# Performance work log

Hardware: AMD Instinct MI355X
Metric: run time of the kernel (lower is better)

## Reference

```python
import jax, jax.numpy as jnp
import numpy as np

B, C, H, S, E, NH, DD, DS = 16, 256, 1024, 1024, 512, 8, 512, 64
HD = E // NH               # head dim = 64
REL_MAX = 2048             # seq_len + prediction_length
S1 = S + 1                 # dyn tokens + 1 static token
NEG = jnp.float32(-1e9)


def setup_inputs() -> dict:
    key = jax.random.key(0)
    ks = jax.random.split(key, 24)
    rn = lambda k, shp, s=0.02: (jax.random.normal(k, shp, jnp.float32) * s)
    return {
        # forward tensor args
        "x":      jax.random.normal(ks[0], (B, C, H), jnp.float32),
        "dyn":    jax.random.normal(ks[1], (B, S, DD), jnp.float32),
        "static": jax.random.normal(ks[2], (B, DS), jnp.float32),
        # dynamic/static encoders (nn.Linear: y = x @ W.T + b)
        "dyn_W":  rn(ks[3], (E, DD)),  "dyn_b":  jnp.zeros((E,), jnp.float32),
        "stat_W": rn(ks[4], (E, DS)),  "stat_b": jnp.zeros((E,), jnp.float32),
        # static FiLM MLP: Linear(E,E) -> LeakyReLU(0.1) -> Linear(E,C) -> Tanh
        "film_W1": rn(ks[5], (E, E)), "film_b1": jnp.zeros((E,), jnp.float32),
        "film_W2": rn(ks[6], (C, E)), "film_b2": jnp.zeros((C,), jnp.float32),
        # query_proj: Conv1d(C->E, k=1)  (weight stored as [E, C])
        "q_W": rn(ks[7], (E, C)), "q_b": jnp.zeros((E,), jnp.float32),
        # MultiheadAttention packed in-proj [3E, E] and out-proj [E, E]
        "in_proj_W": rn(ks[8], (3 * E, E)), "in_proj_b": jnp.zeros((3 * E,), jnp.float32),
        "out_W": rn(ks[9], (E, E)), "out_b": jnp.zeros((E,), jnp.float32),
        # context_proj: Conv1d(E->C, k=1) (weight stored as [C, E])
        "ctx_W": rn(ks[10], (C, E)), "ctx_b": jnp.zeros((C,), jnp.float32),
        # learned relative-position bias table, size 2*REL_MAX-1
        "bias_table": rn(ks[11], (2 * REL_MAX - 1,)),
    }


def _leaky(v):
    return jnp.where(v >= 0, v, 0.1 * v)


def _attn_mask(bias_table):
    """Fused relative-position bias + causal mask, shape [H, S1]."""
    q_ids = jnp.arange(H)[:, None]           # [H,1]
    k_ids = jnp.arange(S1)[None, :]          # [1,S1]
    rel = jnp.clip(q_ids - k_ids, -REL_MAX + 1, REL_MAX - 1)
    bias = bias_table[rel + REL_MAX - 1]     # [H,S1]
    # dynamic tokens: query q may attend dyn token j only if j <= min(q, S-1);
    # last (static) token always visible
    allowed = jnp.minimum(q_ids, S - 1)
    blocked = (k_ids < S) & (k_ids > allowed)
    return bias + jnp.where(blocked, NEG, 0.0)


def reference(x, dyn, static, dyn_W, dyn_b, stat_W, stat_b,
              film_W1, film_b1, film_W2, film_b2, q_W, q_b,
              in_proj_W, in_proj_b, out_W, out_b, ctx_W, ctx_b, bias_table):
    # encoders
    dyn_tokens = dyn @ dyn_W.T + dyn_b                      # [B,S,E]
    static_token = static @ stat_W.T + stat_b               # [B,E]
    film = jnp.tanh(_leaky(static_token @ film_W1.T + film_b1) @ film_W2.T + film_b2)  # [B,C]
    cond_tokens = jnp.concatenate([dyn_tokens, static_token[:, None, :]], axis=1)      # [B,S1,E]

    # query_proj (1x1 conv) : [B,C,H] -> [B,H,E]
    query = jnp.einsum('bch,ec->bhe', x, q_W) + q_b

    # multi-head cross-attention with additive mask
    Wq, Wk, Wv = in_proj_W[:E], in_proj_W[E:2 * E], in_proj_W[2 * E:]
    bq, bk, bv = in_proj_b[:E], in_proj_b[E:2 * E], in_proj_b[2 * E:]
    q = (query @ Wq.T + bq).reshape(B, H, NH, HD).transpose(0, 2, 1, 3)        # [B,NH,H,HD]
    k = (cond_tokens @ Wk.T + bk).reshape(B, S1, NH, HD).transpose(0, 2, 1, 3)  # [B,NH,S1,HD]
    v = (cond_tokens @ Wv.T + bv).reshape(B, S1, NH, HD).transpose(0, 2, 1, 3)

    mask = _attn_mask(bias_table)                                               # [H,S1]
    scores = jnp.einsum('bnqd,bnkd->bnqk', q, k) / jnp.sqrt(jnp.float32(HD)) + mask
    attn = jax.nn.softmax(scores, axis=-1)
    ctx = jnp.einsum('bnqk,bnkd->bnqd', attn, v)                                # [B,NH,H,HD]
    ctx = ctx.transpose(0, 2, 1, 3).reshape(B, H, E) @ out_W.T + out_b          # [B,H,E]

    cond_context = jnp.swapaxes(ctx, 1, 2)                                      # [B,E,H]
    cond_residual = jnp.einsum('beh,ce->bch', cond_context, ctx_W) + ctx_b[None, :, None]
    scale = (1.0 + film)[:, :, None]                                            # FiLM [B,C,1]
    x_cond = (x + cond_residual) * scale                                        # == x*s + res*s
    return x_cond
```

## Files before the change

kernel.cpp:

```cpp
#include <hip/hip_runtime.h>
#include <cmath>

#define B_  16
#define C_  256
#define H_  1024
#define S_  1024
#define E_  512
#define NH_ 8
#define DD_ 512
#define DS_ 64
#define HD_ 64
#define S1_ 1025
#define RELM 2048
#define SV  1032

typedef __attribute__((ext_vector_type(8))) short bf16x8;
typedef __attribute__((ext_vector_type(4))) float f32x4;

__device__ __forceinline__ unsigned short f2bf(float f) {
    unsigned u = __float_as_uint(f);
    u += 0x7fffu + ((u >> 16) & 1u);
    return (unsigned short)(u >> 16);
}

__device__ __forceinline__ void gl2lds16(const unsigned short* g, unsigned short* l) {
#if __has_builtin(__builtin_amdgcn_global_load_lds)
    __builtin_amdgcn_global_load_lds(
        (const __attribute__((address_space(1))) void*)g,
        (__attribute__((address_space(3))) void*)l, 16, 0, 0);
#else
    const int ln = threadIdx.x & 63;
    *(bf16x8*)(l + ln * 8) = *(const bf16x8*)g;
#endif
}

__device__ __forceinline__ void conv8(const float* __restrict__ src,
                                      unsigned short* __restrict__ dst, int i) {
    float4 a = *(const float4*)(src + i);
    float4 b = *(const float4*)(src + i + 4);
    bf16x8 o;
    ((unsigned short*)&o)[0] = f2bf(a.x); ((unsigned short*)&o)[1] = f2bf(a.y);
    ((unsigned short*)&o)[2] = f2bf(a.z); ((unsigned short*)&o)[3] = f2bf(a.w);
    ((unsigned short*)&o)[4] = f2bf(b.x); ((unsigned short*)&o)[5] = f2bf(b.y);
    ((unsigned short*)&o)[6] = f2bf(b.z); ((unsigned short*)&o)[7] = f2bf(b.w);
    *(bf16x8*)(dst + i) = o;
}

__device__ __forceinline__ float wred(float p) {
#pragma unroll
    for (int off = 32; off; off >>= 1) p += __shfl_down(p, off, 64);
    return p;
}

#define U_DYN 1048576
#define U_KV  1114112
#define U_Q   1146880
#define U_TOT 1163264
__global__ __launch_bounds__(512)
void prep_conv(const float* __restrict__ dyn, unsigned short* __restrict__ dyn16,
               const float* __restrict__ ipW, unsigned short* __restrict__ ipWq16,
               unsigned short* __restrict__ ipWkv16,
               const float* __restrict__ ctxW, unsigned short* __restrict__ ctxW16,
               const float* __restrict__ statIn,
               const float* __restrict__ stat_W, const float* __restrict__ stat_b,
               float* __restrict__ st_g, unsigned short* __restrict__ st16)
{
    const int blk = blockIdx.x;
    const int t = threadIdx.x;
    if (blk < 512) {
        const float* ipWkv = ipW + (size_t)E_ * E_;
        const int stride = 512 * 512;
        for (int u = blk * 512 + t; u < U_TOT; u += stride) {
            if (u < U_DYN)      conv8(dyn,   dyn16,   u * 8);
            else if (u < U_KV)  conv8(ipWkv, ipWkv16, (u - U_DYN) * 8);
            else if (u < U_Q)   conv8(ipW,   ipWq16,  (u - U_KV) * 8);
            else                conv8(ctxW,  ctxW16,  (u - U_Q) * 8);
        }
    } else {
        const int sub = blk - 512;
        const int b = sub >> 2;
        const int q = sub & 3;
        const int wv = t >> 6;
        const int ln = t & 63;
        const float sv = statIn[b * DS_ + ln];
#pragma unroll 4
        for (int i = 0; i < 16; i++) {
            const int r = q * 128 + wv * 16 + i;
            const float p = wred(stat_W[(size_t)r * DS_ + ln] * sv);
            if (ln == 0) {
                const float v = p + stat_b[r];
                st_g[(size_t)b * E_ + r] = v;
                st16[(size_t)b * E_ + r] = f2bf(v);
            }
        }
    }
}

__global__ __launch_bounds__(512)
void prep_misc(const float* __restrict__ ipW, const float* __restrict__ ipb,
               const float* __restrict__ ctxW,
               const float* __restrict__ q_W, unsigned short* __restrict__ qWT16,
               const float* __restrict__ dynW, unsigned short* __restrict__ dynWT16,
               const float* __restrict__ outW, unsigned short* __restrict__ outWT16,
               const float* __restrict__ q_b, float* __restrict__ qb2,
               const float* __restrict__ dyn_b, float* __restrict__ bkv2,
               const float* __restrict__ out_b, const float* __restrict__ ctx_b,
               float* __restrict__ cb2,
               const float* __restrict__ st_g,
               const float* __restrict__ fW1, const float* __restrict__ fb1,
               float* __restrict__ h1_g)
{
    __shared__ float tle[64][65];
    const int blk = blockIdx.x;
    const int t = threadIdx.x;
    const float* ipWkv = ipW + (size_t)E_ * E_;
    const float* ipbkv = ipb + E_;

    if (blk < 128) {
        const int b   = blk >> 3;
        const int oct = blk & 7;
        const int wv  = t >> 6;
        const int ln  = t & 63;
        float str[8];
        *(float4*)&str[0] = *(const float4*)&st_g[(size_t)b * E_ + ln * 8];
        *(float4*)&str[4] = *(const float4*)&st_g[(size_t)b * E_ + ln * 8 + 4];
#pragma unroll 2
        for (int i = 0; i < 8; i++) {
            const int r = oct * 64 + wv * 8 + i;
            const float* wr = fW1 + (size_t)r * E_ + ln * 8;
            const float4 a = *(const float4*)wr;
            const float4 c = *(const float4*)(wr + 4);
            float p = a.x * str[0] + a.y * str[1] + a.z * str[2] + a.w * str[3]
                    + c.x * str[4] + c.y * str[5] + c.z * str[6] + c.w * str[7];
            p = wred(p);
            if (ln == 0) {
                const float v = p + fb1[r];
                h1_g[(size_t)b * E_ + r] = (v >= 0.f) ? v : 0.1f * v;
            }
        }
    } else if (blk < 352) {
        const int row = (blk - 128) * 8 + (t >> 6);
        const int ln  = t & 63;
        const float* src; const float* vec; float bias; float* dst;
        if (row < 512)       { src = ipW + (size_t)row * E_;            vec = q_b;   bias = ipb[row];        dst = qb2 + row; }
        else if (row < 1536) { const int n = row - 512;  src = ipWkv + (size_t)n * E_; vec = dyn_b; bias = ipbkv[n]; dst = bkv2 + n; }
        else                 { const int n = row - 1536; src = ctxW + (size_t)n * E_;  vec = out_b; bias = ctx_b[n]; dst = cb2 + n; }
        const float4 a  = *(const float4*)(src + ln * 8);
        const float4 c  = *(const float4*)(src + ln * 8 + 4);
        const float4 va = *(const float4*)(vec + ln * 8);
        const float4 vc = *(const float4*)(vec + ln * 8 + 4);
        float p = a.x * va.x + a.y * va.y + a.z * va.z + a.w * va.w
                + c.x * vc.x + c.y * vc.y + c.z * vc.z + c.w * vc.w;
        p = wred(p);
        if (ln == 0) *dst = p + bias;
    } else {
        const float* src; unsigned short* dst; int R, Cc, tile;
        const int tt = blk - 352;
        if (tt < 32)      { src = q_W;  dst = qWT16;   R = 512; Cc = 256; tile = tt; }
        else if (tt < 96) { src = dynW; dst = dynWT16; R = 512; Cc = 512; tile = tt - 32; }
        else              { src = outW; dst = outWT16; R = 512; Cc = 512; tile = tt - 96; }
        const int tpr = Cc / 64;
        const int r0 = (tile / tpr) * 64;
        const int c0 = (tile % tpr) * 64;
        const int tx = t & 15, ty = t >> 4;
#pragma unroll
        for (int i = 0; i < 2; i++) {
            const float4 v = *(const float4*)&src[(size_t)(r0 + ty + i * 32) * Cc + c0 + tx * 4];
            tle[ty + i * 32][tx * 4 + 0] = v.x;
            tle[ty + i * 32][tx * 4 + 1] = v.y;
            tle[ty + i * 32][tx * 4 + 2] = v.z;
            tle[ty + i * 32][tx * 4 + 3] = v.w;
        }
        __syncthreads();
#pragma unroll
        for (int i = 0; i < 2; i++) {
            const int cc = ty + i * 32;
            ushort4 o;
            o.x = f2bf(tle[tx * 4 + 0][cc]);
            o.y = f2bf(tle[tx * 4 + 1][cc]);
            o.z = f2bf(tle[tx * 4 + 2][cc]);
            o.w = f2bf(tle[tx * 4 + 3][cc]);
            *(ushort4*)&dst[(size_t)(c0 + cc) * R + r0 + tx * 4] = o;
        }
    }
}

__global__ __launch_bounds__(256)
void gemm_fold3(const unsigned short* __restrict__ ipWq16, const unsigned short* __restrict__ qWT16,
                unsigned short* __restrict__ WqW16,
                const unsigned short* __restrict__ ipWkv16, const unsigned short* __restrict__ dynWT16,
                unsigned short* __restrict__ Wkv216,
                const unsigned short* __restrict__ ctxW16, const unsigned short* __restrict__ outWT16,
                unsigned short* __restrict__ M216,
                const float* __restrict__ h1_g,
                const float* __restrict__ fW2, const float* __restrict__ fb2,
                float* __restrict__ scaleB)
{
    __shared__ unsigned short At[128 * 32];
    __shared__ unsigned short Wt[128 * 32];
    const int bid = blockIdx.x;
    const int tid  = threadIdx.x;
    if (bid >= 48) {
        const int sub = bid - 48;
        const int b = sub >> 2;
        const int q = sub & 3;
        const int wv = tid >> 6;
        const int ln = tid & 63;
        float h1r[8];
        *(float4*)&h1r[0] = *(const float4*)&h1_g[(size_t)b * E_ + ln * 8];
        *(float4*)&h1r[4] = *(const float4*)&h1_g[(size_t)b * E_ + ln * 8 + 4];
#pragma unroll 2
        for (int i = 0; i < 16; i++) {
            const int c = q * 64 + wv * 16 + i;
            const float* wr = fW2 + (size_t)c * E_ + ln * 8;
            const float4 a = *(const float4*)wr;
            const float4 cc = *(const float4*)(wr + 4);
            float p = a.x * h1r[0] + a.y * h1r[1] + a.z * h1r[2] + a.w * h1r[3]
                    + cc.x * h1r[4] + cc.y * h1r[5] + cc.z * h1r[6] + cc.w * h1r[7];
            p = wred(p);
            if (ln == 0) scaleB[b * C_ + c] = 1.f + tanhf(p + fb2[c]);
        }
        return;
    }
    const unsigned short *A, *W; unsigned short* O; int N, mb, nb;
    if (bid < 8)       { A = ipWq16;  W = qWT16;   O = WqW16;  N = 256; mb = bid >> 1;       nb = bid & 1; }
    else if (bid < 40) { A = ipWkv16; W = dynWT16; O = Wkv216; N = 512; mb = (bid - 8) >> 2; nb = (bid - 8) & 3; }
    else               { A = ctxW16;  W = outWT16; O = M216;   N = 512; mb = (bid - 40) >> 2; nb = (bid - 40) & 3; }
    const int m0 = mb * 128, n0 = nb * 128;

    const int wave = tid >> 6;
    const int lane = tid & 63;
    const int quad = lane >> 4;
    const int l15  = lane & 15;
    const int rw = (wave >> 1) * 64;
    const int cw = (wave & 1) * 64;
    const int srow = lane >> 2;
    const int scol = (lane & 3) * 8;

    f32x4 acc[4][4] = {};
    for (int k0 = 0; k0 < 512; k0 += 32) {
        __syncthreads();
#pragma unroll
        for (int c = 0; c < 2; c++) {
            const int chunk = wave + c * 4;
            gl2lds16(A + (size_t)(m0 + chunk * 16 + srow) * 512 + k0 + scol, &At[chunk * 512]);
            gl2lds16(W + (size_t)(n0 + chunk * 16 + srow) * 512 + k0 + scol, &Wt[chunk * 512]);
        }
        __syncthreads();
        bf16x8 af[4], wf[4];
#pragma unroll
        for (int i = 0; i < 4; i++)
            af[i] = *(const bf16x8*)&At[(rw + i * 16 + l15) * 32 + quad * 8];
#pragma unroll
        for (int j = 0; j < 4; j++)
            wf[j] = *(const bf16x8*)&Wt[(cw + j * 16 + l15) * 32 + quad * 8];
#pragma unroll
        for (int i = 0; i < 4; i++)
#pragma unroll
            for (int j = 0; j < 4; j++)
                acc[i][j] = __builtin_amdgcn_mfma_f32_16x16x32_bf16(af[i], wf[j], acc[i][j], 0, 0, 0);
    }
#pragma unroll
    for (int i = 0; i < 4; i++)
#pragma unroll
        for (int r = 0; r < 4; r++) {
            const int mm = m0 + rw + i * 16 + quad * 4 + r;
            unsigned short* cp = O + (size_t)mm * N + n0 + cw + l15;
#pragma unroll
            for (int j = 0; j < 4; j++)
                cp[j * 16] = f2bf(acc[i][j][r]);
        }
}

__global__ __launch_bounds__(256)
void xpose_kernel(const float* __restrict__ x, unsigned short* __restrict__ xT)
{
    __shared__ float t[64][65];
    const int b = blockIdx.z;
    const int h0 = blockIdx.x * 64;
    const int c0 = blockIdx.y * 64;
    const int tx = threadIdx.x & 15;
    const int ty = threadIdx.x >> 4;
#pragma unroll
    for (int i = 0; i < 4; i++) {
        const float4 v = *(const float4*)&x[((size_t)(b * C_ + c0 + ty + i * 16)) * H_ + h0 + tx * 4];
        t[ty + i * 16][tx * 4 + 0] = v.x;
        t[ty + i * 16][tx * 4 + 1] = v.y;
        t[ty + i * 16][tx * 4 + 2] = v.z;
        t[ty + i * 16][tx * 4 + 3] = v.w;
    }
    __syncthreads();
#pragma unroll
    for (int i = 0; i < 4; i++) {
        const int hh = ty + i * 16;
        ushort4 o;
        o.x = f2bf(t[tx * 4 + 0][hh]);
        o.y = f2bf(t[tx * 4 + 1][hh]);
        o.z = f2bf(t[tx * 4 + 2][hh]);
        o.w = f2bf(t[tx * 4 + 3][hh]);
        *(ushort4*)&xT[((size_t)(b * H_ + h0 + hh)) * C_ + c0 + tx * 4] = o;
    }
}

template<bool FINAL>
__global__ __launch_bounds__(256)
void gemm_mfma(const unsigned short* __restrict__ A, const unsigned short* __restrict__ W,
               const float* __restrict__ bias, void* __restrict__ Cout,
               int M, int N, int K,
               const float* __restrict__ x, const float* __restrict__ scale)
{
    __shared__ unsigned short At[128 * 32];
    __shared__ unsigned short Wt[128 * 32];
    const int tid  = threadIdx.x;
    const int wave = tid >> 6;
    const int lane = tid & 63;
    const int quad = lane >> 4;
    const int l15  = lane & 15;
    const int m0 = blockIdx.y * 128;
    const int n0 = blockIdx.x * 128;
    const int rw = (wave >> 1) * 64;
    const int cw = (wave & 1) * 64;
    const int zb = FINAL ? blockIdx.z : 0;
    const unsigned short* Wb = FINAL ? W + (size_t)zb * N * K : W;

    const int srow = lane >> 2;
    const int scol = (lane & 3) * 8;

    f32x4 acc[4][4] = {};

    for (int k0 = 0; k0 < K; k0 += 32) {
        __syncthreads();
#pragma unroll
        for (int c = 0; c < 2; c++) {
            const int chunk = wave + c * 4;
            gl2lds16(A  + (size_t)(m0 + chunk * 16 + srow) * K + k0 + scol, &At[chunk * 512]);
            gl2lds16(Wb + (size_t)(n0 + chunk * 16 + srow) * K + k0 + scol, &Wt[chunk * 512]);
        }
        __syncthreads();
        bf16x8 af[4], wf[4];
#pragma unroll
        for (int i = 0; i < 4; i++)
            af[i] = *(const bf16x8*)&At[(rw + i * 16 + l15) * 32 + quad * 8];
#pragma unroll
        for (int j = 0; j < 4; j++)
            wf[j] = *(const bf16x8*)&Wt[(cw + j * 16 + l15) * 32 + quad * 8];
#pragma unroll
        for (int i = 0; i < 4; i++)
#pragma unroll
            for (int j = 0; j < 4; j++)
                acc[i][j] = __builtin_amdgcn_mfma_f32_16x16x32_bf16(af[i], wf[j], acc[i][j], 0, 0, 0);
    }

    if constexpr (!FINAL) {
        float bias4[4];
#pragma unroll
        for (int j = 0; j < 4; j++) bias4[j] = bias[n0 + cw + j * 16 + l15];
#pragma unroll
        for (int i = 0; i < 4; i++) {
#pragma unroll
            for (int r = 0; r < 4; r++) {
                const int mm = m0 + rw + i * 16 + quad * 4 + r;
                if (mm < M) {
                    unsigned short* cp = (unsigned short*)Cout + (size_t)mm * N + n0 + cw + l15;
#pragma unroll
                    for (int j = 0; j < 4; j++)
                        cp[j * 16] = f2bf(acc[i][j][r] + bias4[j]);
                }
            }
        }
    } else {
#pragma unroll
        for (int i = 0; i < 4; i++) {
#pragma unroll
            for (int r = 0; r < 4; r++) {
                const int mm = m0 + rw + i * 16 + quad * 4 + r;
                const float cb = bias[mm];
                const float sc = scale[zb * C_ + mm];
                const size_t base = ((size_t)(zb * C_ + mm)) * H_ + n0 + cw + l15;
#pragma unroll
                for (int j = 0; j < 4; j++)
                    ((float*)Cout)[base + j * 16] = (x[base + j * 16] + acc[i][j][r] + cb) * sc;
            }
        }
    }
}

__global__ __launch_bounds__(256)
void gemm_kv(const unsigned short* __restrict__ dynA, const unsigned short* __restrict__ stA,
             const unsigned short* __restrict__ Wdyn, const unsigned short* __restrict__ Wst,
             const float* __restrict__ bdyn, const float* __restrict__ bst,
             unsigned short* __restrict__ k16, unsigned short* __restrict__ vtmp)
{
    __shared__ unsigned short At[128 * 32];
    __shared__ unsigned short Wt[128 * 32];
    const bool stat = (blockIdx.y == 128);
    const unsigned short* A = stat ? stA : dynA;
    const unsigned short* W = stat ? Wst : Wdyn;
    const float* bias = stat ? bst : bdyn;
    const int m0 = stat ? 0 : blockIdx.y * 128;
    const int n0 = blockIdx.x * 128;

    const int tid  = threadIdx.x;
    const int wave = tid >> 6;
    const int lane = tid & 63;
    const int quad = lane >> 4;
    const int l15  = lane & 15;
    const int rw = (wave >> 1) * 64;
    const int cw = (wave & 1) * 64;
    const int srow = lane >> 2;
    const int scol = (lane & 3) * 8;

    f32x4 acc[4][4] = {};
    for (int k0 = 0; k0 < 512; k0 += 32) {
        __syncthreads();
#pragma unroll
        for (int c = 0; c < 2; c++) {
            const int chunk = wave + c * 4;
            gl2lds16(A + (size_t)(m0 + chunk * 16 + srow) * 512 + k0 + scol, &At[chunk * 512]);
            gl2lds16(W + (size_t)(n0 + chunk * 16 + srow) * 512 + k0 + scol, &Wt[chunk * 512]);
        }
        __syncthreads();
        bf16x8 af[4], wf[4];
#pragma unroll
        for (int i = 0; i < 4; i++)
            af[i] = *(const bf16x8*)&At[(rw + i * 16 + l15) * 32 + quad * 8];
#pragma unroll
        for (int j = 0; j < 4; j++)
            wf[j] = *(const bf16x8*)&Wt[(cw + j * 16 + l15) * 32 + quad * 8];
#pragma unroll
        for (int i = 0; i < 4; i++)
#pragma unroll
            for (int j = 0; j < 4; j++)
                acc[i][j] = __builtin_amdgcn_mfma_f32_16x16x32_bf16(af[i], wf[j], acc[i][j], 0, 0, 0);
    }

    const bool isV = (n0 >= 512);
    unsigned short* base = isV ? vtmp : k16;
    const int c0 = (isV ? n0 - 512 : n0) + cw + l15;
    float bias4[4];
#pragma unroll
    for (int j = 0; j < 4; j++) bias4[j] = bias[n0 + cw + j * 16 + l15];
#pragma unroll
    for (int i = 0; i < 4; i++) {
#pragma unroll
        for (int r = 0; r < 4; r++) {
            const int am = m0 + rw + i * 16 + quad * 4 + r;
            if (!stat || am < 16) {
                const int orow = stat ? (am * S1_ + S_) : ((am >> 10) * S1_ + (am & 1023));
                unsigned short* cp = base + (size_t)orow * 512 + c0;
#pragma unroll
                for (int j = 0; j < 4; j++)
                    cp[j * 16] = f2bf(acc[i][j][r] + bias4[j]);
            }
        }
    }
}

__global__ __launch_bounds__(256)
void vtrans_kernel(const unsigned short* __restrict__ vtmp, unsigned short* __restrict__ vT)
{
    __shared__ unsigned short tle[64][72];
    const int b = blockIdx.z;
    const int s0 = blockIdx.x * 64;
    const int d0 = blockIdx.y * 64;
    const int tx = threadIdx.x & 15;
    const int ty = threadIdx.x >> 4;
#pragma unroll
    for (int i = 0; i < 4; i++) {
        const int s = s0 + ty + i * 16;
        ushort4 v = {0, 0, 0, 0};
        if (s < S1_)
            v = *(const ushort4*)&vtmp[((size_t)(b * S1_ + s)) * 512 + d0 + tx * 4];
        tle[ty + i * 16][tx * 4 + 0] = v.x;
        tle[ty + i * 16][tx * 4 + 1] = v.y;
        tle[ty + i * 16][tx * 4 + 2] = v.z;
        tle[ty + i * 16][tx * 4 + 3] = v.w;
    }
    __syncthreads();
    if (s0 + tx * 4 < SV) {
#pragma unroll
        for (int i = 0; i < 4; i++) {
            const int dd = ty + i * 16;
            ushort4 o;
            o.x = tle[tx * 4 + 0][dd];
            o.y = tle[tx * 4 + 1][dd];
            o.z = tle[tx * 4 + 2][dd];
            o.w = tle[tx * 4 + 3][dd];
            *(ushort4*)&vT[((size_t)(b * 512 + d0 + dd)) * SV + s0 + tx * 4] = o;
        }
    }
}

#define KS 72
#define VTS 40
#define PS 40

__global__ __launch_bounds__(256)
void attn_mfma_kernel(const unsigned short* __restrict__ q,
                      const unsigned short* __restrict__ k16,
                      const unsigned short* __restrict__ vT,
                      const float* __restrict__ bt,
                      unsigned short* __restrict__ ctx)
{
    const int blk  = blockIdx.x;
    const int qt   = 7 - (blk >> 7);
    const int pair = blk & 127;
    const int nh   = pair & 7;
    const int b    = pair >> 3;
    const int tid  = threadIdx.x;
    const int wave = tid >> 6;
    const int lane = tid & 63;
    const int quad = lane >> 4;
    const int l15  = lane & 15;
    const int q0w  = qt * 128 + wave * 32;

    __shared__ unsigned short Kt[32 * KS];
    __shared__ unsigned short VTl[64 * VTS];
    __shared__ unsigned short Pt[4][16 * PS];
    __shared__ float btl[2048];

    for (int i = tid; i < 2048; i += 256) btl[i] = bt[1023 + i];

    bf16x8 qa[2][2];
    const size_t qbase = ((size_t)(b * H_ + q0w)) * E_ + nh * HD_;
#pragma unroll
    for (int qf = 0; qf < 2; qf++)
#pragma unroll
        for (int ch = 0; ch < 2; ch++)
            qa[qf][ch] = *(const bf16x8*)(q + qbase + (size_t)(qf * 16 + l15) * E_ + ch * 32 + quad * 8);

    bf16x8 ones;
#pragma unroll
    for (int j = 0; j < 8; j++) ((short*)&ones)[j] = (short)0x3F80;

    f32x4 o[2][4] = {};
    f32x4 lf[2] = {};
    bf16x8 pa[2];

    const int srow = tid >> 3;
    const int scol = (tid & 7) * 8;
    const int frow = tid >> 2;
    const int fcol = (tid & 3) * 8;
    const unsigned short* vrow = vT + ((size_t)(b * 512 + nh * HD_ + frow)) * SV;
    const int ntiles = 4 * qt + 5;

    for (int t = 0; t < ntiles; t++) {
        const int k0 = (t == ntiles - 1) ? 1024 : t * 32;
        __syncthreads();
        {
            *(bf16x8*)&Kt[srow * KS + scol] =
                *(const bf16x8*)(k16 + ((size_t)(b * S1_) + k0 + srow) * 512 + nh * HD_ + scol);
            *(bf16x8*)&VTl[frow * VTS + fcol] = *(const bf16x8*)(vrow + k0 + fcol);
        }
        __syncthreads();

        f32x4 s[2][2] = {};
#pragma unroll
        for (int ch = 0; ch < 2; ch++) {
            const bf16x8 kb0 = *(const bf16x8*)&Kt[l15 * KS + ch * 32 + quad * 8];
            const bf16x8 kb1 = *(const bf16x8*)&Kt[(16 + l15) * KS + ch * 32 + quad * 8];
            s[0][0] = __builtin_amdgcn_mfma_f32_16x16x32_bf16(qa[0][ch], kb0, s[0][0], 0, 0, 0);
            s[1][0] = __builtin_amdgcn_mfma_f32_16x16x32_bf16(qa[1][ch], kb0, s[1][0], 0, 0, 0);
            s[0][1] = __builtin_amdgcn_mfma_f32_16x16x32_bf16(qa[0][ch], kb1, s[0][1], 0, 0, 0);
            s[1][1] = __builtin_amdgcn_mfma_f32_16x16x32_bf16(qa[1][ch], kb1, s[1][1], 0, 0, 0);
        }
#pragma unroll
        for (int qf = 0; qf < 2; qf++) {
            unsigned short* pw = Pt[wave];
#pragma unroll
            for (int f = 0; f < 2; f++) {
                const int kk = k0 + f * 16 + l15;
#pragma unroll
                for (int r = 0; r < 4; r++) {
                    const int qi = q0w + qf * 16 + quad * 4 + r;
                    const bool vis = (kk <= qi) || (kk == 1024);
                    const float pp = vis ? __expf(s[qf][f][r] * 0.125f + btl[qi - kk + 1024]) : 0.f;
                    pw[(quad * 4 + r) * PS + f * 16 + l15] = f2bf(pp);
                }
            }
            pa[qf] = *(const bf16x8*)&pw[l15 * PS + quad * 8];
        }

#pragma unroll
        for (int qf = 0; qf < 2; qf++)
            lf[qf] = __builtin_amdgcn_mfma_f32_16x16x32_bf16(pa[qf], ones, lf[qf], 0, 0, 0);
#pragma unroll
        for (int dt = 0; dt < 4; dt++) {
            const bf16x8 vb = *(const bf16x8*)&VTl[(dt * 16 + l15) * VTS + quad * 8];
#pragma unroll
            for (int qf = 0; qf < 2; qf++)
                o[qf][dt] = __builtin_amdgcn_mfma_f32_16x16x32_bf16(pa[qf], vb, o[qf][dt], 0, 0, 0);
        }
    }

#pragma unroll
    for (int qf = 0; qf < 2; qf++) {
        unsigned short* crow = ctx + ((size_t)(b * H_ + q0w + qf * 16 + quad * 4)) * E_ + nh * HD_ + l15;
#pragma unroll
        for (int r = 0; r < 4; r++) {
            const float inv = 1.f / lf[qf][r];
#pragma unroll
            for (int dt = 0; dt < 4; dt++)
                crow[(size_t)r * E_ + dt * 16] = f2bf(o[qf][dt][r] * inv);
        }
    }
}

extern "C" void kernel_launch(void* const* d_in, const int* in_sizes, int n_in,
                              void* d_out, int out_size, void* d_ws, size_t ws_size,
                              hipStream_t stream)
{
    (void)in_sizes; (void)n_in; (void)out_size; (void)ws_size;
    const float* x      = (const float*)d_in[0];
    const float* dyn    = (const float*)d_in[1];
    const float* statIn = (const float*)d_in[2];
    const float* dyn_W  = (const float*)d_in[3];
    const float* dyn_b  = (const float*)d_in[4];
    const float* stat_W = (const float*)d_in[5];
    const float* stat_b = (const float*)d_in[6];
    const float* fW1    = (const float*)d_in[7];
    const float* fb1    = (const float*)d_in[8];
    const float* fW2    = (const float*)d_in[9];
    const float* fb2    = (const float*)d_in[10];
    const float* q_W    = (const float*)d_in[11];
    const float* q_b    = (const float*)d_in[12];
    const float* ipW    = (const float*)d_in[13];
    const float* ipb    = (const float*)d_in[14];
    const float* out_W  = (const float*)d_in[15];
    const float* out_b  = (const float*)d_in[16];
    const float* ctx_W  = (const float*)d_in[17];
    const float* ctx_b  = (const float*)d_in[18];
    const float* bt     = (const float*)d_in[19];
    float* out = (float*)d_out;
    const float* ipbkv = ipb + E_;

    const size_t KV_ROWS = 16512;
    char* w = (char*)d_ws; size_t off = 0;
    unsigned short* k16   = (unsigned short*)(w + off); off += KV_ROWS * 512 * 2;
    unsigned short* vtmp  = (unsigned short*)(w + off); off += KV_ROWS * 512 * 2;
    unsigned short* dyn16 = (unsigned short*)(w + off); off += (size_t)16 * 512 * SV * 2;
    unsigned short* q16   = (unsigned short*)(w + off); off += (size_t)B_ * H_ * E_ * 2;
    unsigned short* xT16  = (unsigned short*)(w + off); off += (size_t)B_ * H_ * C_ * 2;
    unsigned short* st16    = (unsigned short*)(w + off); off += (size_t)128 * E_ * 2;
    unsigned short* Wkv216  = (unsigned short*)(w + off); off += (size_t)1024 * 512 * 2;
    unsigned short* ipWkv16 = (unsigned short*)(w + off); off += (size_t)1024 * 512 * 2;
    unsigned short* ipWq16  = (unsigned short*)(w + off); off += (size_t)512 * 512 * 2;
    unsigned short* ctxW16  = (unsigned short*)(w + off); off += (size_t)256 * 512 * 2;
    unsigned short* qWT16   = (unsigned short*)(w + off); off += (size_t)256 * 512 * 2;
    unsigned short* dynWT16 = (unsigned short*)(w + off); off += (size_t)512 * 512 * 2;
    unsigned short* outWT16 = (unsigned short*)(w + off); off += (size_t)512 * 512 * 2;
    unsigned short* WqW16   = (unsigned short*)(w + off); off += (size_t)E_ * C_ * 2;
    unsigned short* M216    = (unsigned short*)(w + off); off += (size_t)C_ * E_ * 2;
    float* scaleB = (float*)(w + off); off += (size_t)B_ * C_ * 4;
    float* qb2    = (float*)(w + off); off += E_ * 4;
    float* bkv2   = (float*)(w + off); off += 1024 * 4;
    float* cb2    = (float*)(w + off); off += C_ * 4;
    float* st_g   = (float*)(w + off); off += (size_t)B_ * E_ * 4;
    float* h1_g   = (float*)(w + off); off += (size_t)B_ * E_ * 4;
    unsigned short* vT16  = dyn16;
    unsigned short* ctx16 = vtmp;

    prep_conv<<<576, 512, 0, stream>>>(dyn, dyn16, ipW, ipWq16, ipWkv16, ctx_W, ctxW16,
                                       statIn, stat_W, stat_b, st_g, st16);
    prep_misc<<<512, 512, 0, stream>>>(ipW, ipb, ctx_W, q_W, qWT16, dyn_W, dynWT16,
                                       out_W, outWT16, q_b, qb2, dyn_b, bkv2,
                                       out_b, ctx_b, cb2,
                                       st_g, fW1, fb1, h1_g);
    gemm_fold3<<<112, 256, 0, stream>>>(ipWq16, qWT16, WqW16,
                                        ipWkv16, dynWT16, Wkv216,
                                        ctxW16, outWT16, M216,
                                        h1_g, fW2, fb2, scaleB);
    xpose_kernel<<<dim3(H_ / 64, C_ / 64, B_), 256, 0, stream>>>(x, xT16);
    gemm_mfma<false><<<dim3(E_ / 128, B_ * H_ / 128), 256, 0, stream>>>(
        xT16, WqW16, qb2, q16, B_ * H_, E_, C_, nullptr, nullptr);
    gemm_kv<<<dim3(1024 / 128, 129), 256, 0, stream>>>(
        dyn16, st16, Wkv216, ipWkv16, bkv2, ipbkv, k16, vtmp);
    vtrans_kernel<<<dim3(17, 8, B_), 256, 0, stream>>>(vtmp, vT16);
    attn_mfma_kernel<<<1024, 256, 0, stream>>>(q16, k16, vT16, bt, ctx16);
    gemm_mfma<true><<<dim3(H_ / 128, C_ / 128, B_), 256, 0, stream>>>(
        M216, ctx16, cb2, out, C_, H_, E_, x, scaleB);
}
```

Baseline: 284.4 us.

## Fold causal mask into bias table, use exp2, and swizzle P tile

The attention kernel now builds a prescaled bias table in LDS: negative relative offsets hold -1e9 and the rest are multiplied by log2(e). This lets the inner loop drop the per-element visibility test and call a native exp2 with a fused scale. The final static-token tile gets its own path that keeps the special visibility rule. P-tile writes to and reads from LDS use an XOR column swizzle to cut bank conflicts. The cost is a duplicated code path and reliance on exp2 of very negative values flushing to zero.

```diff
diff --git a/kernel.cpp b/kernel.cpp
--- a/kernel.cpp
+++ b/kernel.cpp
@@ -22,6 +22,12 @@
     u += 0x7fffu + ((u >> 16) & 1u);
     return (unsigned short)(u >> 16);
 }
+
+#if __has_builtin(__builtin_amdgcn_exp2f)
+#define EXP2F(x) __builtin_amdgcn_exp2f(x)
+#else
+#define EXP2F(x) exp2f(x)
+#endif
 
 __device__ __forceinline__ void gl2lds16(const unsigned short* g, unsigned short* l) {
 #if __has_builtin(__builtin_amdgcn_global_load_lds)
@@ -519,7 +525,10 @@
     __shared__ unsigned short Pt[4][16 * PS];
     __shared__ float btl[2048];
 
-    for (int i = tid; i < 2048; i += 256) btl[i] = bt[1023 + i];
+    for (int i = tid; i < 2048; i += 256)
+        btl[i] = (i < 1024) ? -1.0e9f : bt[1023 + i] * 1.442695041f;
+
+    const float c2 = 0.125f * 1.442695041f;
 
     bf16x8 qa[2][2];
     const size_t qbase = ((size_t)(b * H_ + q0w)) * E_ + nh * HD_;
@@ -543,6 +552,9 @@
     const int fcol = (tid & 3) * 8;
     const unsigned short* vrow = vT + ((size_t)(b * 512 + nh * HD_ + frow)) * SV;
     const int ntiles = 4 * qt + 5;
+    const int wblk0 = (l15 >> 3);
+    const int wsub  = (l15 & 7);
+    const int rblk  = (quad ^ ((l15 >> 2) & 3)) << 3;
 
     for (int t = 0; t < ntiles; t++) {
         const int k0 = (t == ntiles - 1) ? 1024 : t * 32;
@@ -564,21 +576,41 @@
             s[0][1] = __builtin_amdgcn_mfma_f32_16x16x32_bf16(qa[0][ch], kb1, s[0][1], 0, 0, 0);
             s[1][1] = __builtin_amdgcn_mfma_f32_16x16x32_bf16(qa[1][ch], kb1, s[1][1], 0, 0, 0);
         }
-#pragma unroll
-        for (int qf = 0; qf < 2; qf++) {
-            unsigned short* pw = Pt[wave];
-#pragma unroll
-            for (int f = 0; f < 2; f++) {
-                const int kk = k0 + f * 16 + l15;
-#pragma unroll
-                for (int r = 0; r < 4; r++) {
-                    const int qi = q0w + qf * 16 + quad * 4 + r;
-                    const bool vis = (kk <= qi) || (kk == 1024);
-                    const float pp = vis ? __expf(s[qf][f][r] * 0.125f + btl[qi - kk + 1024]) : 0.f;
-                    pw[(quad * 4 + r) * PS + f * 16 + l15] = f2bf(pp);
+
+        if (t != ntiles - 1) {
+#pragma unroll
+            for (int qf = 0; qf < 2; qf++) {
+                unsigned short* pw = Pt[wave];
+#pragma unroll
+                for (int f = 0; f < 2; f++) {
+                    const int base = q0w + qf * 16 + quad * 4 - (k0 + f * 16 + l15) + 1024;
+                    const int cswz = ((f * 2 + wblk0) ^ quad) * 8 + wsub;
+#pragma unroll
+                    for (int r = 0; r < 4; r++) {
+                        const float pp = EXP2F(s[qf][f][r] * c2 + btl[base + r]);
+                        pw[(quad * 4 + r) * PS + cswz] = f2bf(pp);
+                    }
                 }
+                pa[qf] = *(const bf16x8*)&pw[l15 * PS + rblk];
             }
-            pa[qf] = *(const bf16x8*)&pw[l15 * PS + quad * 8];
+        } else {
+#pragma unroll
+            for (int qf = 0; qf < 2; qf++) {
+                unsigned short* pw = Pt[wave];
+#pragma unroll
+                for (int f = 0; f < 2; f++) {
+                    const int kk = k0 + f * 16 + l15;
+                    const int cswz = ((f * 2 + wblk0) ^ quad) * 8 + wsub;
+#pragma unroll
+                    for (int r = 0; r < 4; r++) {
+                        const int qi = q0w + qf * 16 + quad * 4 + r;
+                        const float pp = (kk == 1024)
+                            ? __expf(s[qf][f][r] * 0.125f + bt[1023 + qi]) : 0.f;
+                        pw[(quad * 4 + r) * PS + cswz] = f2bf(pp);
+                    }
+                }
+                pa[qf] = *(const bf16x8*)&pw[l15 * PS + rblk];
+            }
         }
 
 #pragma unroll
```

New measurement: 282.8 us. Within noise of the previous version (-0.5%).
